# Kernel tuning notes

Measured on AMD Instinct MI355X. Metric: run time of the kernel, lower is better.

Reference implementation:

```python
import jax, jax.numpy as jnp
import numpy as np

MAX_DISP = 4  # matches init_kwargs


def setup_inputs() -> dict:
    key = jax.random.key(0)
    k1, k2 = jax.random.split(key)
    fmap1 = jax.random.normal(k1, (8, 256, 64, 128), dtype=jnp.float32)
    fmap2 = jax.random.normal(k2, (8, 256, 64, 128), dtype=jnp.float32)
    return {"fmap1": fmap1, "fmap2": fmap2}


def reference(fmap1, fmap2):
    # corr(x,y,dx,dy) = sum_c fmap1[c,y,x] * fmap2[c,y+dy,x+dx]
    pad = MAX_DISP
    B, C, H, W = fmap1.shape
    f2p = jnp.pad(fmap2, ((0, 0), (0, 0), (pad, pad), (pad, pad)))
    side = 2 * pad + 1  # 9 -> 81 displacements total
    # Loop over the small fixed set of 81 static displacements; each term is a
    # fused elementwise-multiply + channel reduction (einsum over c).
    corrs = [
        jnp.einsum('bchw,bchw->bhw', fmap1, f2p[:, :, y0:y0 + H, x0:x0 + W])
        for y0 in range(side)
        for x0 in range(side)
    ]
    return jnp.stack(corrs, axis=1)  # (B, 81, H, W)
```

## Files before the change

kernel.cpp:

```cpp
#include <hip/hip_runtime.h>


namespace {
constexpr int B_ = 8, C_ = 256, H_ = 64, W_ = 128;
constexpr int SIDE = 9, ND = 81, PAD = 4;
constexpr int HW = H_ * W_;
constexpr int KC = 32, NCH = C_ / KC;
constexpr int YB = 8, RWS = YB + 2 * PAD;
constexpr int XB = 16;
constexpr int NQ = 4;
constexpr int YP_ = H_ + 2 * PAD;
constexpr int XP_ = 144;
constexpr size_t ROWU = (size_t)NQ * XP_;
constexpr size_t PERB = (size_t)NCH * YP_ * ROWU;
constexpr size_t NW2 = (size_t)B_ * PERB;
constexpr size_t WS_BYTES = NW2 * 16;
constexpr int TILE_U4 = RWS * NQ * 32;
}

typedef __attribute__((ext_vector_type(8))) short short8;
typedef __attribute__((ext_vector_type(4))) float float4v;
typedef __attribute__((address_space(1))) void gvoid;
typedef __attribute__((address_space(3))) void svoid;

__device__ __forceinline__ unsigned bf16rne(float f) {
  unsigned u = __float_as_uint(f);
  return (u + 0x7fffu + ((u >> 16) & 1u)) >> 16;
}
__device__ __forceinline__ unsigned packbf2(float lo, float hi) {
  return bf16rne(lo) | (bf16rne(hi) << 16);
}

__global__ __launch_bounds__(256)
void cvt_f2(const float* __restrict__ f2, uint4* __restrict__ w2) {
  const int id = blockIdx.x;
  const int b = id & 7;
  const int e2 = (id >> 3) * 256 + (int)threadIdx.x;
  const int xp2 = e2 % (XP_ / 2);
  int r = e2 / (XP_ / 2);
  const int q = r & 3;
  r >>= 2;
  const int yp = r % YP_;
  const int cs = r / YP_;
  const int xp = 2 * xp2;
  const int yg = yp - PAD, xg = xp - PAD;
  uint4 o0 = {0u, 0u, 0u, 0u}, o1 = o0;
  if (yg >= 0 && yg < H_ && xg >= 0 && xg <= W_ - 2) {
    const float* s =
        f2 + ((size_t)(b * C_ + cs * KC + q * 8) * H_ + yg) * W_ + xg;
    const float2 v0 = *(const float2*)(s + 0 * HW);
    const float2 v1 = *(const float2*)(s + 1 * HW);
    const float2 v2 = *(const float2*)(s + 2 * HW);
    const float2 v3 = *(const float2*)(s + 3 * HW);
    const float2 v4 = *(const float2*)(s + 4 * HW);
    const float2 v5 = *(const float2*)(s + 5 * HW);
    const float2 v6 = *(const float2*)(s + 6 * HW);
    const float2 v7 = *(const float2*)(s + 7 * HW);
    o0.x = packbf2(v0.x, v1.x);  o1.x = packbf2(v0.y, v1.y);
    o0.y = packbf2(v2.x, v3.x);  o1.y = packbf2(v2.y, v3.y);
    o0.z = packbf2(v4.x, v5.x);  o1.z = packbf2(v4.y, v5.y);
    o0.w = packbf2(v6.x, v7.x);  o1.w = packbf2(v6.y, v7.y);
  }
  const size_t e = (((size_t)(cs * YP_ + yp) * NQ + q) * XP_) + xp;
  uint4* d = w2 + (size_t)b * PERB + e;
  d[0] = o0;
  d[1] = o1;
}

__global__ __launch_bounds__(512, 4)
void corr_mfma2(const float* __restrict__ f1, const uint4* __restrict__ w2,
                float* __restrict__ out) {
  __shared__ uint4 f2s[2 * TILE_U4];

  const int id = blockIdx.x;
  const int b = id & 7;
  const int k = id >> 3;
  const int xg = k & 7, yg = k >> 3;
  const int x0 = xg * XB, y0 = yg * YB;

  const int t = threadIdx.x, lane = t & 63, w = t >> 6;
  const int v = lane & 15, q = lane >> 4;
  const int sq = q << 1;
  const int l_hi = lane >> 5;
  const int l_xq = lane & 31;

  const uint4* w2b = w2 + (size_t)b * PERB;
  const float* f1b = f1 + (size_t)b * C_ * HW;

  auto issue_stage = [&](int ch, int buf) {
    const uint4* wc = w2b + (size_t)ch * ((size_t)YP_ * ROWU);
#pragma unroll
    for (int kk = 0; kk < 4; ++kk) {
      const int r = 2 * w + (kk >> 1);
      const int qp = kk & 1;
      const int qq = 2 * qp + l_hi;
      const int xqs = l_xq ^ (qq << 1);
      const uint4* gp = wc + (size_t)(y0 + r) * ROWU + (size_t)qq * XP_ + x0 + xqs;
      uint4* lp = &f2s[buf * TILE_U4 + (r * NQ + qp * 2) * 32];
      __builtin_amdgcn_global_load_lds((gvoid*)gp, (svoid*)lp, 16, 0, 0);
    }
  };
  auto issue_f1 = [&](int ch, float* p) {
    const float* fp =
        f1b + ((size_t)(ch * KC + q * 8) * H_ + (y0 + w)) * W_ + x0 + v;
#pragma unroll
    for (int j = 0; j < 8; ++j) p[j] = fp[(size_t)j * HW];
  };

  float4v acc[SIDE][2];
#pragma unroll
  for (int i = 0; i < SIDE; ++i) {
    acc[i][0] = (float4v){0.f, 0.f, 0.f, 0.f};
    acc[i][1] = (float4v){0.f, 0.f, 0.f, 0.f};
  }

  float pbuf[3][8];
  issue_stage(0, 0);
  __builtin_amdgcn_sched_barrier(0);
  issue_f1(0, pbuf[0]);
  __builtin_amdgcn_sched_barrier(0);
  issue_stage(1, 1);
  __builtin_amdgcn_sched_barrier(0);
  issue_f1(1, pbuf[1]);
  __builtin_amdgcn_sched_barrier(0);

#pragma unroll
  for (int ch = 0; ch < NCH; ++ch) {
    float* pc = pbuf[ch % 3];
    uint4 afu;
    afu.x = packbf2(pc[0], pc[1]);
    afu.y = packbf2(pc[2], pc[3]);
    afu.z = packbf2(pc[4], pc[5]);
    afu.w = packbf2(pc[6], pc[7]);
    const short8 af = __builtin_bit_cast(short8, afu);

    asm volatile("s_waitcnt vmcnt(12)" ::: "memory");
    __builtin_amdgcn_sched_barrier(0);
    __builtin_amdgcn_s_barrier();
    __builtin_amdgcn_sched_barrier(0);

    const int bo = (ch & 1) * TILE_U4;
    __builtin_amdgcn_s_setprio(1);
#pragma unroll
    for (int dy = 0; dy < SIDE; ++dy) {
      const uint4* base = &f2s[bo + ((w + dy) * NQ + q) * 32];
      const short8 b0 = __builtin_bit_cast(short8, base[v ^ sq]);
      const short8 b1 = __builtin_bit_cast(short8, base[(v + 16) ^ sq]);
      acc[dy][0] =
          __builtin_amdgcn_mfma_f32_16x16x32_bf16(af, b0, acc[dy][0], 0, 0, 0);
      acc[dy][1] =
          __builtin_amdgcn_mfma_f32_16x16x32_bf16(af, b1, acc[dy][1], 0, 0, 0);
    }
    __builtin_amdgcn_s_setprio(0);
    __builtin_amdgcn_sched_barrier(0);
    __builtin_amdgcn_s_barrier();
    __builtin_amdgcn_sched_barrier(0);
    if (ch + 2 < NCH) {
      issue_stage(ch + 2, ch & 1);
      __builtin_amdgcn_sched_barrier(0);
      issue_f1(ch + 2, pbuf[(ch + 2) % 3]);
      __builtin_amdgcn_sched_barrier(0);
    }
  }

  const int y = y0 + w;
  float* outb = out + (size_t)b * ND * HW + (size_t)y * W_ + x0;
#pragma unroll
  for (int dy = 0; dy < SIDE; ++dy) {
#pragma unroll
    for (int r = 0; r < 4; ++r) {
      const int m = q * 4 + r;
      const int dx0 = v - m;
      if (dx0 >= 0 && dx0 <= 8)
        outb[(size_t)(dy * SIDE + dx0) * HW + m] = acc[dy][0][r];
      const int dx1 = v - m + 16;
      if (dx1 <= 8)
        outb[(size_t)(dy * SIDE + dx1) * HW + m] = acc[dy][1][r];
    }
  }
}

namespace fb {
constexpr int PXS = 20, F2PX = 32, F2U = 16 * (F2PX / 4) * 16;
}

__global__ __launch_bounds__(512, 4)
void corr_fb(const float* __restrict__ f1, const float* __restrict__ f2,
             float* __restrict__ out) {
  using namespace fb;
  __shared__ __align__(16) unsigned f2s[RWS * F2PX * PXS];
  __shared__ __align__(16) unsigned f1s[YB * XB * PXS];

  const int id = blockIdx.x;
  const int b = id & 7;
  const int k = id >> 3;
  const int xg = k & 7, yg = k >> 3;
  const int x0 = xg * XB, y0 = yg * YB;
  const int t = threadIdx.x, lane = t & 63, w = t >> 6;
  const int v = lane & 15, q = lane >> 4;

  float4v acc[SIDE][2];
#pragma unroll
  for (int i = 0; i < SIDE; ++i) {
    acc[i][0] = (float4v){0.f, 0.f, 0.f, 0.f};
    acc[i][1] = (float4v){0.f, 0.f, 0.f, 0.f};
  }
  const float* __restrict__ f1b = f1 + (size_t)b * C_ * HW;
  const float* __restrict__ f2b = f2 + (size_t)b * C_ * HW;

  for (int ch = 0; ch < NCH; ++ch) {
    const int c0 = ch * KC;
    if (ch) __syncthreads();
#pragma unroll
    for (int u0 = 0; u0 < F2U; u0 += 512) {
      const int u = u0 + t;
      const int cp = u & 15;
      const int t2 = u >> 4;
      const int pxq = t2 & 7;
      const int r = t2 >> 3;
      const int ygl = y0 - PAD + r;
      const int xb = x0 - PAD + pxq * 4;
      float4 va = make_float4(0.f, 0.f, 0.f, 0.f), vb = va;
      if (ygl >= 0 && ygl < H_ && xb >= 0 && xb <= W_ - 4) {
        const float* p = f2b + ((size_t)(c0 + 2 * cp) * H_ + ygl) * W_ + xb;
        va = *(const float4*)p;
        vb = *(const float4*)(p + HW);
      }
      unsigned* d = &f2s[(r * F2PX + pxq * 4) * PXS + cp];
      d[0 * PXS] = packbf2(va.x, vb.x);
      d[1 * PXS] = packbf2(va.y, vb.y);
      d[2 * PXS] = packbf2(va.z, vb.z);
      d[3 * PXS] = packbf2(va.w, vb.w);
    }
    {
      const int cp = t & 15;
      const int t2 = t >> 4;
      const int pxq = t2 & 3;
      const int r = t2 >> 2;
      const float* p =
          f1b + ((size_t)(c0 + 2 * cp) * H_ + (y0 + r)) * W_ + x0 + pxq * 4;
      const float4 va = *(const float4*)p;
      const float4 vb = *(const float4*)(p + HW);
      unsigned* d = &f1s[(r * XB + pxq * 4) * PXS + cp];
      d[0 * PXS] = packbf2(va.x, vb.x);
      d[1 * PXS] = packbf2(va.y, vb.y);
      d[2 * PXS] = packbf2(va.z, vb.z);
      d[3 * PXS] = packbf2(va.w, vb.w);
    }
    __syncthreads();

    const short8 af = __builtin_bit_cast(
        short8, *(const uint4*)&f1s[(w * XB + v) * PXS + 4 * q]);
#pragma unroll
    for (int dy = 0; dy < SIDE; ++dy) {
      const unsigned* fp = &f2s[((w + dy) * F2PX + v) * PXS + 4 * q];
      const short8 b0 = __builtin_bit_cast(short8, *(const uint4*)fp);
      const short8 b1 =
          __builtin_bit_cast(short8, *(const uint4*)(fp + 16 * PXS));
      acc[dy][0] =
          __builtin_amdgcn_mfma_f32_16x16x32_bf16(af, b0, acc[dy][0], 0, 0, 0);
      acc[dy][1] =
          __builtin_amdgcn_mfma_f32_16x16x32_bf16(af, b1, acc[dy][1], 0, 0, 0);
    }
  }
  const int y = y0 + w;
  float* outb = out + (size_t)b * ND * HW + (size_t)y * W_ + x0;
#pragma unroll
  for (int dy = 0; dy < SIDE; ++dy) {
#pragma unroll
    for (int r = 0; r < 4; ++r) {
      const int m = q * 4 + r;
      const int dx0 = v - m;
      if (dx0 >= 0 && dx0 <= 8)
        outb[(size_t)(dy * SIDE + dx0) * HW + m] = acc[dy][0][r];
      const int dx1 = v - m + 16;
      if (dx1 <= 8)
        outb[(size_t)(dy * SIDE + dx1) * HW + m] = acc[dy][1][r];
    }
  }
}

extern "C" void kernel_launch(void* const* d_in, const int* in_sizes, int n_in,
                              void* d_out, int out_size, void* d_ws,
                              size_t ws_size, hipStream_t stream) {
  (void)in_sizes; (void)n_in; (void)out_size;
  const float* f1 = (const float*)d_in[0];
  const float* f2 = (const float*)d_in[1];
  float* out = (float*)d_out;
  if (ws_size >= WS_BYTES) {
    uint4* w2 = (uint4*)d_ws;
    cvt_f2<<<dim3((unsigned)(NW2 / 512)), 256, 0, stream>>>(f2, w2);
    corr_mfma2<<<dim3(512), 512, 0, stream>>>(f1, w2, out);
  } else {
    corr_fb<<<dim3(512), 512, 0, stream>>>(f1, f2, out);
  }
}
```

Measured before the change: 183.0 us.

## Split dy range across two blocks, triple-buffer f2 tiles, preload f1 fragments

Each output tile is now handled by two blocks, one taking dy 0-4 and the other dy 5-8, which doubles the grid to 1024 blocks. Each block stages 12 padded rows per channel chunk instead of 16. The f2 shared-memory staging moves from double to triple buffering, so the prefetch for chunk ch+2 is issued right after the barrier and the second barrier per iteration is dropped. All f1 fragments are loaded and packed to bf16 into registers before the main loop. This is meant to raise parallelism and shorten the per-block serial chain. The costs are loading the f1 data twice across the two halves, extra register pressure from the 8 preloaded fragments, and an imbalanced last dy group, since one half does 5 rows and the other 4.

```diff
diff --git a/kernel.cpp b/kernel.cpp
--- a/kernel.cpp
+++ b/kernel.cpp
@@ -6,8 +6,7 @@
 constexpr int SIDE = 9, ND = 81, PAD = 4;
 constexpr int HW = H_ * W_;
 constexpr int KC = 32, NCH = C_ / KC;
-constexpr int YB = 8, RWS = YB + 2 * PAD;
-constexpr int XB = 16;
+constexpr int YB = 8, XB = 16;
 constexpr int NQ = 4;
 constexpr int YP_ = H_ + 2 * PAD;
 constexpr int XP_ = 144;
@@ -15,7 +14,8 @@
 constexpr size_t PERB = (size_t)NCH * YP_ * ROWU;
 constexpr size_t NW2 = (size_t)B_ * PERB;
 constexpr size_t WS_BYTES = NW2 * 16;
-constexpr int TILE_U4 = RWS * NQ * 32;
+constexpr int RSTG = 12;
+constexpr int TILE_U4 = RSTG * NQ * 32;
 }
 
 typedef __attribute__((ext_vector_type(8))) short short8;
@@ -68,15 +68,19 @@
 }
 
 __global__ __launch_bounds__(512, 4)
-void corr_mfma2(const float* __restrict__ f1, const uint4* __restrict__ w2,
+void corr_mfma3(const float* __restrict__ f1, const uint4* __restrict__ w2,
                 float* __restrict__ out) {
-  __shared__ uint4 f2s[2 * TILE_U4];
+  __shared__ uint4 f2s[3 * TILE_U4];
 
   const int id = blockIdx.x;
   const int b = id & 7;
   const int k = id >> 3;
-  const int xg = k & 7, yg = k >> 3;
+  const int xg = k & 7;
+  const int half = (k >> 3) & 1;
+  const int yg = k >> 4;
   const int x0 = xg * XB, y0 = yg * YB;
+  const int y0r = y0 + 5 * half;
+  const int ndy = 5 - half;
 
   const int t = threadIdx.x, lane = t & 63, w = t >> 6;
   const int v = lane & 15, q = lane >> 4;
@@ -90,98 +94,108 @@
   auto issue_stage = [&](int ch, int buf) {
     const uint4* wc = w2b + (size_t)ch * ((size_t)YP_ * ROWU);
 #pragma unroll
-    for (int kk = 0; kk < 4; ++kk) {
-      const int r = 2 * w + (kk >> 1);
-      const int qp = kk & 1;
+    for (int kk = 0; kk < 3; ++kk) {
+      const int g = w * 3 + kk;
+      const int r = g >> 1, qp = g & 1;
+      int rs = y0r + r;
+      rs = rs > YP_ - 1 ? YP_ - 1 : rs;
       const int qq = 2 * qp + l_hi;
       const int xqs = l_xq ^ (qq << 1);
-      const uint4* gp = wc + (size_t)(y0 + r) * ROWU + (size_t)qq * XP_ + x0 + xqs;
+      const uint4* gp = wc + (size_t)rs * ROWU + (size_t)qq * XP_ + x0 + xqs;
       uint4* lp = &f2s[buf * TILE_U4 + (r * NQ + qp * 2) * 32];
       __builtin_amdgcn_global_load_lds((gvoid*)gp, (svoid*)lp, 16, 0, 0);
     }
   };
-  auto issue_f1 = [&](int ch, float* p) {
-    const float* fp =
-        f1b + ((size_t)(ch * KC + q * 8) * H_ + (y0 + w)) * W_ + x0 + v;
-#pragma unroll
-    for (int j = 0; j < 8; ++j) p[j] = fp[(size_t)j * HW];
-  };
-
-  float4v acc[SIDE][2];
-#pragma unroll
-  for (int i = 0; i < SIDE; ++i) {
+
+  uint4 af8[NCH];
+  {
+    const float* fb = f1b + ((size_t)(q * 8) * H_ + (y0 + w)) * W_ + x0 + v;
+    float ta[8], tb[8];
+#pragma unroll
+    for (int j = 0; j < 8; ++j) ta[j] = fb[(size_t)j * HW];
+#pragma unroll
+    for (int c = 0; c < NCH; ++c) {
+      float* cur = (c & 1) ? tb : ta;
+      float* nxt = (c & 1) ? ta : tb;
+      if (c + 1 < NCH) {
+#pragma unroll
+        for (int j = 0; j < 8; ++j)
+          nxt[j] = fb[(size_t)((c + 1) * KC + j) * HW];
+      }
+      uint4 u;
+      u.x = packbf2(cur[0], cur[1]);
+      u.y = packbf2(cur[2], cur[3]);
+      u.z = packbf2(cur[4], cur[5]);
+      u.w = packbf2(cur[6], cur[7]);
+      af8[c] = u;
+    }
+  }
+
+  float4v acc[5][2];
+#pragma unroll
+  for (int i = 0; i < 5; ++i) {
     acc[i][0] = (float4v){0.f, 0.f, 0.f, 0.f};
     acc[i][1] = (float4v){0.f, 0.f, 0.f, 0.f};
   }
 
-  float pbuf[3][8];
   issue_stage(0, 0);
-  __builtin_amdgcn_sched_barrier(0);
-  issue_f1(0, pbuf[0]);
-  __builtin_amdgcn_sched_barrier(0);
   issue_stage(1, 1);
   __builtin_amdgcn_sched_barrier(0);
-  issue_f1(1, pbuf[1]);
-  __builtin_amdgcn_sched_barrier(0);
 
 #pragma unroll
   for (int ch = 0; ch < NCH; ++ch) {
-    float* pc = pbuf[ch % 3];
-    uint4 afu;
-    afu.x = packbf2(pc[0], pc[1]);
-    afu.y = packbf2(pc[2], pc[3]);
-    afu.z = packbf2(pc[4], pc[5]);
-    afu.w = packbf2(pc[6], pc[7]);
-    const short8 af = __builtin_bit_cast(short8, afu);
-
-    asm volatile("s_waitcnt vmcnt(12)" ::: "memory");
+    if (ch == NCH - 1)
+      asm volatile("s_waitcnt vmcnt(0)" ::: "memory");
+    else
+      asm volatile("s_waitcnt vmcnt(3)" ::: "memory");
     __builtin_amdgcn_sched_barrier(0);
     __builtin_amdgcn_s_barrier();
     __builtin_amdgcn_sched_barrier(0);
 
-    const int bo = (ch & 1) * TILE_U4;
+    if (ch + 2 < NCH) issue_stage(ch + 2, (ch + 2) % 3);
+    __builtin_amdgcn_sched_barrier(0);
+
+    const int bo = (ch % 3) * TILE_U4;
+    const short8 af = __builtin_bit_cast(short8, af8[ch]);
     __builtin_amdgcn_s_setprio(1);
 #pragma unroll
-    for (int dy = 0; dy < SIDE; ++dy) {
-      const uint4* base = &f2s[bo + ((w + dy) * NQ + q) * 32];
-      const short8 b0 = __builtin_bit_cast(short8, base[v ^ sq]);
-      const short8 b1 = __builtin_bit_cast(short8, base[(v + 16) ^ sq]);
-      acc[dy][0] =
-          __builtin_amdgcn_mfma_f32_16x16x32_bf16(af, b0, acc[dy][0], 0, 0, 0);
-      acc[dy][1] =
-          __builtin_amdgcn_mfma_f32_16x16x32_bf16(af, b1, acc[dy][1], 0, 0, 0);
+    for (int i = 0; i < 5; ++i) {
+      if (i < ndy) {
+        const uint4* base = &f2s[bo + ((w + i) * NQ + q) * 32];
+        const short8 b0 = __builtin_bit_cast(short8, base[v ^ sq]);
+        const short8 b1 = __builtin_bit_cast(short8, base[(v + 16) ^ sq]);
+        acc[i][0] = __builtin_amdgcn_mfma_f32_16x16x32_bf16(af, b0, acc[i][0],
+                                                            0, 0, 0);
+        acc[i][1] = __builtin_amdgcn_mfma_f32_16x16x32_bf16(af, b1, acc[i][1],
+                                                            0, 0, 0);
+      }
     }
     __builtin_amdgcn_s_setprio(0);
     __builtin_amdgcn_sched_barrier(0);
-    __builtin_amdgcn_s_barrier();
-    __builtin_amdgcn_sched_barrier(0);
-    if (ch + 2 < NCH) {
-      issue_stage(ch + 2, ch & 1);
-      __builtin_amdgcn_sched_barrier(0);
-      issue_f1(ch + 2, pbuf[(ch + 2) % 3]);
-      __builtin_amdgcn_sched_barrier(0);
-    }
   }
 
   const int y = y0 + w;
   float* outb = out + (size_t)b * ND * HW + (size_t)y * W_ + x0;
 #pragma unroll
-  for (int dy = 0; dy < SIDE; ++dy) {
-#pragma unroll
-    for (int r = 0; r < 4; ++r) {
-      const int m = q * 4 + r;
-      const int dx0 = v - m;
-      if (dx0 >= 0 && dx0 <= 8)
-        outb[(size_t)(dy * SIDE + dx0) * HW + m] = acc[dy][0][r];
-      const int dx1 = v - m + 16;
-      if (dx1 <= 8)
-        outb[(size_t)(dy * SIDE + dx1) * HW + m] = acc[dy][1][r];
+  for (int i = 0; i < 5; ++i) {
+    if (i < ndy) {
+      const int dyg = half * 5 + i;
+#pragma unroll
+      for (int r = 0; r < 4; ++r) {
+        const int m = q * 4 + r;
+        const int dx0 = v - m;
+        if (dx0 >= 0 && dx0 <= 8)
+          outb[(size_t)(dyg * SIDE + dx0) * HW + m] = acc[i][0][r];
+        const int dx1 = v - m + 16;
+        if (dx1 <= 8)
+          outb[(size_t)(dyg * SIDE + dx1) * HW + m] = acc[i][1][r];
+      }
     }
   }
 }
 
 namespace fb {
-constexpr int PXS = 20, F2PX = 32, F2U = 16 * (F2PX / 4) * 16;
+constexpr int PXS = 20, F2PX = 32, RWS = 16, F2U = RWS * (F2PX / 4) * 16;
 }
 
 __global__ __launch_bounds__(512, 4)
@@ -290,7 +304,7 @@
   if (ws_size >= WS_BYTES) {
     uint4* w2 = (uint4*)d_ws;
     cvt_f2<<<dim3((unsigned)(NW2 / 512)), 256, 0, stream>>>(f2, w2);
-    corr_mfma2<<<dim3(512), 512, 0, stream>>>(f1, w2, out);
+    corr_mfma3<<<dim3(1024), 512, 0, stream>>>(f1, w2, out);
   } else {
     corr_fb<<<dim3(512), 512, 0, stream>>>(f1, f2, out);
   }
```

New measurement: 197.3 us. 1.08x slower.

## Split correlation work across dy halves with smaller blocks for more parallelism

Applied to the files above, without the earlier changes.

The MFMA correlation kernel now uses 256-thread blocks covering 4 output rows, and splits the 9 vertical displacements into two halves (5 and 4) handled by separate blocks, for 2048 blocks instead of 512. Each block stages only 8 rows of fmap2 per channel chunk, and the f1 prefetch drops from triple to double buffering, issued right after the barrier. The aim is more blocks per CU and fewer accumulator registers, so latency is better hidden. In exchange, fmap1 is loaded twice (once per dy half), fmap2 rows are reloaded more often across blocks, and the wait counts are retuned.

```diff
diff --git a/kernel.cpp b/kernel.cpp
--- a/kernel.cpp
+++ b/kernel.cpp
@@ -6,8 +6,7 @@
 constexpr int SIDE = 9, ND = 81, PAD = 4;
 constexpr int HW = H_ * W_;
 constexpr int KC = 32, NCH = C_ / KC;
-constexpr int YB = 8, RWS = YB + 2 * PAD;
-constexpr int XB = 16;
+constexpr int YB = 4, XB = 16;
 constexpr int NQ = 4;
 constexpr int YP_ = H_ + 2 * PAD;
 constexpr int XP_ = 144;
@@ -15,7 +14,8 @@
 constexpr size_t PERB = (size_t)NCH * YP_ * ROWU;
 constexpr size_t NW2 = (size_t)B_ * PERB;
 constexpr size_t WS_BYTES = NW2 * 16;
-constexpr int TILE_U4 = RWS * NQ * 32;
+constexpr int RSTG = 8;
+constexpr int TILE_U4 = RSTG * NQ * 32;
 }
 
 typedef __attribute__((ext_vector_type(8))) short short8;
@@ -67,16 +67,21 @@
   d[1] = o1;
 }
 
-__global__ __launch_bounds__(512, 4)
-void corr_mfma2(const float* __restrict__ f1, const uint4* __restrict__ w2,
+__global__ __launch_bounds__(256, 5)
+void corr_mfma4(const float* __restrict__ f1, const uint4* __restrict__ w2,
                 float* __restrict__ out) {
   __shared__ uint4 f2s[2 * TILE_U4];
 
   const int id = blockIdx.x;
   const int b = id & 7;
-  const int k = id >> 3;
-  const int xg = k & 7, yg = k >> 3;
-  const int x0 = xg * XB, y0 = yg * YB;
+  const int t2 = id >> 3;
+  const int xg = t2 & 7;
+  const int t3 = t2 >> 3;
+  const int half = t3 & 1;
+  const int ygq = t3 >> 1;
+  const int x0 = xg * XB, y0 = ygq * YB;
+  const int y0r = y0 + 5 * half;
+  const int ndy = 5 - half;
 
   const int t = threadIdx.x, lane = t & 63, w = t >> 6;
   const int v = lane & 15, q = lane >> 4;
@@ -93,9 +98,11 @@
     for (int kk = 0; kk < 4; ++kk) {
       const int r = 2 * w + (kk >> 1);
       const int qp = kk & 1;
+      int rs = y0r + r;
+      rs = rs > YP_ - 1 ? YP_ - 1 : rs;
       const int qq = 2 * qp + l_hi;
       const int xqs = l_xq ^ (qq << 1);
-      const uint4* gp = wc + (size_t)(y0 + r) * ROWU + (size_t)qq * XP_ + x0 + xqs;
+      const uint4* gp = wc + (size_t)rs * ROWU + (size_t)qq * XP_ + x0 + xqs;
       uint4* lp = &f2s[buf * TILE_U4 + (r * NQ + qp * 2) * 32];
       __builtin_amdgcn_global_load_lds((gvoid*)gp, (svoid*)lp, 16, 0, 0);
     }
@@ -107,26 +114,24 @@
     for (int j = 0; j < 8; ++j) p[j] = fp[(size_t)j * HW];
   };
 
-  float4v acc[SIDE][2];
-#pragma unroll
-  for (int i = 0; i < SIDE; ++i) {
+  float4v acc[5][2];
+#pragma unroll
+  for (int i = 0; i < 5; ++i) {
     acc[i][0] = (float4v){0.f, 0.f, 0.f, 0.f};
     acc[i][1] = (float4v){0.f, 0.f, 0.f, 0.f};
   }
 
-  float pbuf[3][8];
+  float p0[8], p1[8];
   issue_stage(0, 0);
   __builtin_amdgcn_sched_barrier(0);
-  issue_f1(0, pbuf[0]);
+  issue_f1(0, p0);
   __builtin_amdgcn_sched_barrier(0);
   issue_stage(1, 1);
   __builtin_amdgcn_sched_barrier(0);
-  issue_f1(1, pbuf[1]);
-  __builtin_amdgcn_sched_barrier(0);
 
 #pragma unroll
   for (int ch = 0; ch < NCH; ++ch) {
-    float* pc = pbuf[ch % 3];
+    float* pc = (ch & 1) ? p1 : p0;
     uint4 afu;
     afu.x = packbf2(pc[0], pc[1]);
     afu.y = packbf2(pc[2], pc[3]);
@@ -134,54 +139,57 @@
     afu.w = packbf2(pc[6], pc[7]);
     const short8 af = __builtin_bit_cast(short8, afu);
 
-    asm volatile("s_waitcnt vmcnt(12)" ::: "memory");
+    asm volatile("s_waitcnt vmcnt(4)" ::: "memory");
     __builtin_amdgcn_sched_barrier(0);
     __builtin_amdgcn_s_barrier();
     __builtin_amdgcn_sched_barrier(0);
 
+    if (ch + 1 < NCH) issue_f1(ch + 1, (ch & 1) ? p0 : p1);
+
     const int bo = (ch & 1) * TILE_U4;
     __builtin_amdgcn_s_setprio(1);
 #pragma unroll
-    for (int dy = 0; dy < SIDE; ++dy) {
-      const uint4* base = &f2s[bo + ((w + dy) * NQ + q) * 32];
-      const short8 b0 = __builtin_bit_cast(short8, base[v ^ sq]);
-      const short8 b1 = __builtin_bit_cast(short8, base[(v + 16) ^ sq]);
-      acc[dy][0] =
-          __builtin_amdgcn_mfma_f32_16x16x32_bf16(af, b0, acc[dy][0], 0, 0, 0);
-      acc[dy][1] =
-          __builtin_amdgcn_mfma_f32_16x16x32_bf16(af, b1, acc[dy][1], 0, 0, 0);
+    for (int i = 0; i < 5; ++i) {
+      if (i < ndy) {
+        const uint4* base = &f2s[bo + ((w + i) * NQ + q) * 32];
+        const short8 b0 = __builtin_bit_cast(short8, base[v ^ sq]);
+        const short8 b1 = __builtin_bit_cast(short8, base[(v + 16) ^ sq]);
+        acc[i][0] = __builtin_amdgcn_mfma_f32_16x16x32_bf16(af, b0, acc[i][0],
+                                                            0, 0, 0);
+        acc[i][1] = __builtin_amdgcn_mfma_f32_16x16x32_bf16(af, b1, acc[i][1],
+                                                            0, 0, 0);
+      }
     }
     __builtin_amdgcn_s_setprio(0);
     __builtin_amdgcn_sched_barrier(0);
     __builtin_amdgcn_s_barrier();
     __builtin_amdgcn_sched_barrier(0);
-    if (ch + 2 < NCH) {
-      issue_stage(ch + 2, ch & 1);
-      __builtin_amdgcn_sched_barrier(0);
-      issue_f1(ch + 2, pbuf[(ch + 2) % 3]);
-      __builtin_amdgcn_sched_barrier(0);
-    }
+    if (ch + 2 < NCH) issue_stage(ch + 2, ch & 1);
   }
 
   const int y = y0 + w;
   float* outb = out + (size_t)b * ND * HW + (size_t)y * W_ + x0;
 #pragma unroll
-  for (int dy = 0; dy < SIDE; ++dy) {
-#pragma unroll
-    for (int r = 0; r < 4; ++r) {
-      const int m = q * 4 + r;
-      const int dx0 = v - m;
-      if (dx0 >= 0 && dx0 <= 8)
-        outb[(size_t)(dy * SIDE + dx0) * HW + m] = acc[dy][0][r];
-      const int dx1 = v - m + 16;
-      if (dx1 <= 8)
-        outb[(size_t)(dy * SIDE + dx1) * HW + m] = acc[dy][1][r];
+  for (int i = 0; i < 5; ++i) {
+    if (i < ndy) {
+      const int dyg = half * 5 + i;
+#pragma unroll
+      for (int r = 0; r < 4; ++r) {
+        const int m = q * 4 + r;
+        const int dx0 = v - m;
+        if (dx0 >= 0 && dx0 <= 8)
+          outb[(size_t)(dyg * SIDE + dx0) * HW + m] = acc[i][0][r];
+        const int dx1 = v - m + 16;
+        if (dx1 <= 8)
+          outb[(size_t)(dyg * SIDE + dx1) * HW + m] = acc[i][1][r];
+      }
     }
   }
 }
 
 namespace fb {
-constexpr int PXS = 20, F2PX = 32, F2U = 16 * (F2PX / 4) * 16;
+constexpr int PXS = 20, F2PX = 32, RWS = 16, F2U = RWS * (F2PX / 4) * 16;
+constexpr int YBf = 8;
 }
 
 __global__ __launch_bounds__(512, 4)
@@ -189,13 +197,13 @@
              float* __restrict__ out) {
   using namespace fb;
   __shared__ __align__(16) unsigned f2s[RWS * F2PX * PXS];
-  __shared__ __align__(16) unsigned f1s[YB * XB * PXS];
+  __shared__ __align__(16) unsigned f1s[YBf * XB * PXS];
 
   const int id = blockIdx.x;
   const int b = id & 7;
   const int k = id >> 3;
   const int xg = k & 7, yg = k >> 3;
-  const int x0 = xg * XB, y0 = yg * YB;
+  const int x0 = xg * XB, y0 = yg * YBf;
   const int t = threadIdx.x, lane = t & 63, w = t >> 6;
   const int v = lane & 15, q = lane >> 4;
 
@@ -290,7 +298,7 @@
   if (ws_size >= WS_BYTES) {
     uint4* w2 = (uint4*)d_ws;
     cvt_f2<<<dim3((unsigned)(NW2 / 512)), 256, 0, stream>>>(f2, w2);
-    corr_mfma2<<<dim3(512), 512, 0, stream>>>(f1, w2, out);
+    corr_mfma4<<<dim3(2048), 256, 0, stream>>>(f1, w2, out);
   } else {
     corr_fb<<<dim3(512), 512, 0, stream>>>(f1, f2, out);
   }
```

Measured after the change: 193.4 us. 5.7% more time.

## Stage output through LDS for coalesced float4 stores and retune prefetch pipeline

Applied to the files above, without the earlier changes.

The epilogue now writes accumulator fragments into shared memory (reusing the f2 tile buffer), then has the block store them to global memory as contiguous float4 rows. This replaces scattered scalar stores that hit 81 separate displacement planes. The fmap1 prefetch drops from triple to double buffering, issued right after the barrier of each step, with a tighter vmcnt wait. The setprio hints are removed. This trades some prefetch depth and extra LDS round-trips for fewer, wider global writes.

```diff
diff --git a/kernel.cpp b/kernel.cpp
--- a/kernel.cpp
+++ b/kernel.cpp
@@ -16,6 +16,7 @@
 constexpr size_t NW2 = (size_t)B_ * PERB;
 constexpr size_t WS_BYTES = NW2 * 16;
 constexpr int TILE_U4 = RWS * NQ * 32;
+constexpr int EPS_SLOTS = ND * YB * XB / 4;
 }
 
 typedef __attribute__((ext_vector_type(8))) short short8;
@@ -114,19 +115,17 @@
     acc[i][1] = (float4v){0.f, 0.f, 0.f, 0.f};
   }
 
-  float pbuf[3][8];
+  float p0[8], p1[8];
   issue_stage(0, 0);
   __builtin_amdgcn_sched_barrier(0);
-  issue_f1(0, pbuf[0]);
+  issue_f1(0, p0);
   __builtin_amdgcn_sched_barrier(0);
   issue_stage(1, 1);
   __builtin_amdgcn_sched_barrier(0);
-  issue_f1(1, pbuf[1]);
-  __builtin_amdgcn_sched_barrier(0);
 
 #pragma unroll
   for (int ch = 0; ch < NCH; ++ch) {
-    float* pc = pbuf[ch % 3];
+    float* pc = (ch & 1) ? p1 : p0;
     uint4 afu;
     afu.x = packbf2(pc[0], pc[1]);
     afu.y = packbf2(pc[2], pc[3]);
@@ -134,13 +133,13 @@
     afu.w = packbf2(pc[6], pc[7]);
     const short8 af = __builtin_bit_cast(short8, afu);
 
-    asm volatile("s_waitcnt vmcnt(12)" ::: "memory");
-    __builtin_amdgcn_sched_barrier(0);
+    asm volatile("s_waitcnt vmcnt(4)" ::: "memory");
     __builtin_amdgcn_s_barrier();
     __builtin_amdgcn_sched_barrier(0);
 
+    if (ch + 1 < NCH) issue_f1(ch + 1, (ch & 1) ? p0 : p1);
+
     const int bo = (ch & 1) * TILE_U4;
-    __builtin_amdgcn_s_setprio(1);
 #pragma unroll
     for (int dy = 0; dy < SIDE; ++dy) {
       const uint4* base = &f2s[bo + ((w + dy) * NQ + q) * 32];
@@ -151,20 +150,14 @@
       acc[dy][1] =
           __builtin_amdgcn_mfma_f32_16x16x32_bf16(af, b1, acc[dy][1], 0, 0, 0);
     }
-    __builtin_amdgcn_s_setprio(0);
     __builtin_amdgcn_sched_barrier(0);
     __builtin_amdgcn_s_barrier();
     __builtin_amdgcn_sched_barrier(0);
-    if (ch + 2 < NCH) {
-      issue_stage(ch + 2, ch & 1);
-      __builtin_amdgcn_sched_barrier(0);
-      issue_f1(ch + 2, pbuf[(ch + 2) % 3]);
-      __builtin_amdgcn_sched_barrier(0);
-    }
-  }
-
-  const int y = y0 + w;
-  float* outb = out + (size_t)b * ND * HW + (size_t)y * W_ + x0;
+    if (ch + 2 < NCH) issue_stage(ch + 2, ch & 1);
+  }
+
+  __builtin_amdgcn_s_barrier();
+  float* eps = (float*)f2s;
 #pragma unroll
   for (int dy = 0; dy < SIDE; ++dy) {
 #pragma unroll
@@ -172,11 +165,20 @@
       const int m = q * 4 + r;
       const int dx0 = v - m;
       if (dx0 >= 0 && dx0 <= 8)
-        outb[(size_t)(dy * SIDE + dx0) * HW + m] = acc[dy][0][r];
-      const int dx1 = v - m + 16;
+        eps[((dy * SIDE + dx0) * YB + w) * XB + m] = acc[dy][0][r];
+      const int dx1 = dx0 + 16;
       if (dx1 <= 8)
-        outb[(size_t)(dy * SIDE + dx1) * HW + m] = acc[dy][1][r];
-    }
+        eps[((dy * SIDE + dx1) * YB + w) * XB + m] = acc[dy][1][r];
+    }
+  }
+  __builtin_amdgcn_s_barrier();
+  float* outp = out + (size_t)b * ND * HW;
+  for (int s = t; s < EPS_SLOTS; s += 512) {
+    const int p = s >> 5;
+    const int yy = (s & 31) >> 2;
+    const int xq = s & 3;
+    const float4 val = *(const float4*)&eps[s * 4];
+    *(float4*)&outp[((size_t)p * H_ + y0 + yy) * W_ + x0 + xq * 4] = val;
   }
 }
 
```

Result: no change. 179.4 us (-1.9%).
